# Kernel optimization log

Measured on AMD Instinct MI355X. Metric: run time of the kernel, lower is better.

Reference implementation:

```python
import jax, jax.numpy as jnp
import numpy as np

H = 1        # hidden_size: torch code branches `if c_0 > 0`, so state is scalar
SPIN = 365   # spinLen
TRAIN = 5000 # traintimeLen
ML = 2.9086
SL = 1.898


def setup_inputs() -> dict:
    key = jax.random.key(0)
    ks = jax.random.split(key, 13)
    B, S, I = 100000, 1, 2
    return {
        "x": jax.random.uniform(ks[0], (B, S, I), dtype=jnp.float32),
        "y_obs": jax.random.uniform(ks[1], (B, 1), dtype=jnp.float32),
        "p_mean": jax.random.uniform(ks[2], (1,), dtype=jnp.float32),
        "p_std": jnp.ones((1,), jnp.float32),
        "weight_r_yom": jax.random.uniform(ks[3], (H, H), dtype=jnp.float32),
        "weight_r_yom_gw": jax.random.uniform(ks[4], (H, H), dtype=jnp.float32),
        "weight_r_ylm": jax.random.uniform(ks[5], (H, H), dtype=jnp.float32),
        "weight_r_yfm": jax.random.uniform(ks[6], (H, H), dtype=jnp.float32),
        "bias_b0_yom": jax.random.uniform(ks[7], (H,), dtype=jnp.float32),
        "weight_b1_yom": jax.random.uniform(ks[8], (H, H), dtype=jnp.float32),
        "bias_b0_yom_gw": jax.random.uniform(ks[9], (H,), dtype=jnp.float32),
        "weight_b1_yom_gw": jax.random.uniform(ks[10], (H, H), dtype=jnp.float32),
        "bias_b0_ylm": jax.random.uniform(ks[11], (H,), dtype=jnp.float32),
        "weight_b2_ylm": jax.random.uniform(ks[12], (H, H), dtype=jnp.float32),
        "epoch": 1,
        "time_lag": 0,
    }


def _forward(x, y_obs, p_mean, p_std,
             weight_r_yom, weight_r_yom_gw, weight_r_ylm, weight_r_yfm,
             bias_b0_yom, weight_b1_yom, bias_b0_yom_gw, weight_b1_yom_gw,
             bias_b0_ylm, weight_b2_ylm, time_lag):
    B, S, _ = x.shape
    # softmax-like weight ratios (step-independent, hoisted out of the loop)
    den = (jnp.exp(weight_r_yom) + jnp.exp(weight_r_yom_gw)
           + jnp.exp(weight_r_ylm) + jnp.exp(weight_r_yfm))
    oo1 = jnp.exp(weight_r_yom) / den      # [H,H]
    oogw1 = jnp.exp(weight_r_yom_gw) / den
    ol1 = jnp.exp(weight_r_ylm) / den
    obsstd = jnp.std(y_obs[SPIN:TRAIN], ddof=1)  # torch.std is unbiased

    # step order in torch: b outer, t inner over x_orig[b, t] (batch_first)
    xs = x[time_lag:].reshape(-1, x.shape[-1])  # [(B-tl)*S, 2]

    def step(c0, u):                        # c0: [1,H]
        u1 = jnp.full((1, H), u[0])         # inflow
        u2 = jnp.full((1, H), u[1])         # PET
        z = (c0 - p_mean) / p_std
        oo = oo1 * jax.nn.sigmoid(bias_b0_yom + z @ weight_b1_yom)
        oogw = oogw1 * jax.nn.sigmoid(bias_b0_yom_gw + z @ weight_b1_yom_gw)
        ol = ol1 * jax.nn.sigmoid(bias_b0_ylm + ((u2 - ML) / SL) @ weight_b2_ylm)
        pos = c0 > 0
        ol_c = jnp.where(pos, ol - jax.nn.relu(ol - u2 / jnp.where(pos, c0, 1.0)), ol)
        f = 1.0 - oo - oogw - ol_c
        c1 = f * c0 + u1                    # ib = 0 => full inflow, bp = 0
        outs = (oo * c0, c0, ol * c0, ol_c * c0, oogw * c0, oo, ol, ol_c, f, oogw)
        return c1, outs

    c0 = jnp.zeros((1, H), x.dtype)
    _, outs = jax.lax.scan(step, c0, xs)

    def per_b(o):  # keep last-t value per b; zero-pad the skipped time_lag rows
        o = o.reshape(B - time_lag, S, 1, H)[:, -1, 0]
        return jnp.concatenate([jnp.zeros((time_lag, H), o.dtype), o], axis=0)

    h_n, c_n, l_n, lc_n, gw_n, g_oo, g_ol, g_olc, g_f, g_oogw = map(per_b, outs)
    zeros = jnp.zeros((B, H), x.dtype)
    bp_n = zeros      # ib = 0 always
    g_ib = zeros
    mask = jnp.concatenate([jnp.zeros((time_lag, H), x.dtype),
                            jnp.ones((B - time_lag, H), x.dtype)], axis=0)
    obs_std = obsstd * mask
    h_nout = jnp.concatenate([h_n, obs_std], axis=1)
    return (h_n, c_n, l_n, lc_n, bp_n, gw_n, g_ib, g_oo, g_ol, g_olc, g_f,
            g_oogw, h_nout, obs_std)


def reference(x, y_obs, p_mean, p_std, weight_r_yom, weight_r_yom_gw,
              weight_r_ylm, weight_r_yfm, bias_b0_yom, weight_b1_yom,
              bias_b0_yom_gw, weight_b1_yom_gw, bias_b0_ylm, weight_b2_ylm,
              epoch, time_lag):
    return _forward(x, y_obs, p_mean, p_std, weight_r_yom, weight_r_yom_gw,
                    weight_r_ylm, weight_r_yfm, bias_b0_yom, weight_b1_yom,
                    bias_b0_yom_gw, weight_b1_yom_gw, bias_b0_ylm,
                    weight_b2_ylm, time_lag)
```

## Files before the change

### kernel.cpp

```cpp
#include <hip/hip_runtime.h>
#include <math.h>


#define SPIN  365
#define TRAIN 5000
#define CHUNK 4
#define WARM  48
#define PF    4
#define BLK   128
#define SPAN  (BLK * CHUNK)
#define TLEN  (SPAN + WARM)
#define TSTR  140

#define F4BASE (SPIN - 1)
#define NF4    ((TRAIN - F4BASE) / 4)
#define SITER  ((NF4 + BLK - 1) / BLK)

#define MLc 2.9086f
#define SLc 1.898f

__device__ __forceinline__ float exp2a(float x) {
    float r; asm("v_exp_f32 %0, %1" : "=v"(r) : "v"(x)); return r;
}
__device__ __forceinline__ float rcpa(float x) {
    float r; asm("v_rcp_f32 %0, %1" : "=v"(r) : "v"(x)); return r;
}

__global__ void __launch_bounds__(BLK)
scan_kernel(const float* __restrict__ x, const float* __restrict__ y,
            const float* __restrict__ p_mean, const float* __restrict__ p_std,
            const float* __restrict__ w_r_yom, const float* __restrict__ w_r_yom_gw,
            const float* __restrict__ w_r_ylm, const float* __restrict__ w_r_yfm,
            const float* __restrict__ b0_yom, const float* __restrict__ w_b1_yom,
            const float* __restrict__ b0_yom_gw, const float* __restrict__ w_b1_yom_gw,
            const float* __restrict__ b0_ylm, const float* __restrict__ w_b2_ylm,
            const int* __restrict__ tlp, float* __restrict__ out, int B) {
    __shared__ __align__(128) float4 tile4[TLEN];
    __shared__ float sred[4];

    const int tid = threadIdx.x;
    const int tl = *tlp;
    const int N = B - tl;
    const size_t Bs = (size_t)B;

    const int blkbase = blockIdx.x * SPAN;
    const bool active = (blkbase < N);

    float2 sx[(TLEN + BLK - 1) / BLK];
    if (active) {
        const int T0 = blkbase - WARM;
        const float2* xp = (const float2*)x + tl;
        const int Nm1 = N - 1;
#pragma unroll
        for (int n = 0; n < (TLEN + BLK - 1) / BLK; ++n) {
            const int k = n * BLK + tid;
            const int g = min(max(T0 + min(k, TLEN - 1), 0), Nm1);
            sx[n] = xp[g];
        }
    }

    float4 yv[SITER];
    {
        const float4* y4 = (const float4*)(y + F4BASE);
#pragma unroll
        for (int n = 0; n < SITER; ++n)
            yv[n] = y4[min(n * BLK + tid, NF4 - 1)];
    }

    for (int r = blockIdx.x * BLK + tid; r < tl; r += gridDim.x * BLK) {
#pragma unroll
        for (int p = 0; p < 12; ++p) out[p * Bs + r] = 0.0f;
        out[12 * Bs + 2 * (size_t)r] = 0.0f;
        out[12 * Bs + 2 * (size_t)r + 1] = 0.0f;
        out[14 * Bs + r] = 0.0f;
    }

    const float pm = p_mean[0], inv_ps = 1.0f / p_std[0];
    const float ea = __expf(w_r_yom[0]);
    const float eb = __expf(w_r_yom_gw[0]);
    const float ec = __expf(w_r_ylm[0]);
    const float ed = __expf(w_r_yfm[0]);
    const float iden = 1.0f / (ea + eb + ec + ed);
    const float oo1 = ea * iden, oogw1 = eb * iden, ol1 = ec * iden;
    const float oo1g = oo1 + oogw1;
    const float LOG2E = 1.4426950408889634f;
    const float m1 = w_b1_yom[0]    * inv_ps, k1 = b0_yom[0]    - pm * m1;
    const float m2 = w_b1_yom_gw[0] * inv_ps, k2 = b0_yom_gw[0] - pm * m2;
    const float m3 = w_b2_ylm[0] * (1.0f / SLc), k3 = b0_ylm[0] - MLc * m3;
    const float A1 = -k1 * LOG2E, M1 = -m1 * LOG2E;
    const float A2 = -k2 * LOG2E, M2 = -m2 * LOG2E;
    const float A3 = -k3 * LOG2E, M3 = -m3 * LOG2E;

    if (active) {
#pragma unroll
        for (int n = 0; n < (TLEN + BLK - 1) / BLK; ++n) {
            const int k = n * BLK + tid;
            if (k < TLEN) {
                const float2 u = sx[n];
                const float olv = ol1 * rcpa(1.0f + exp2a(fmaf(u.y, M3, A3)));
                tile4[(k & 3) * TSTR + (k >> 2)] = make_float4(u.x, olv, u.y, 0.0f);
            }
        }
    }
    __syncthreads();

    float vh[CHUNK], vcc[CHUNK], vl[CHUNK], vlc[CHUNK], vgw[CHUNK];
    float voo[CHUNK], vol[CHUNK], volc[CHUNK], vf[CHUNK], vgg[CHUNK];
    const int i = tid;
    const int s0g = blkbase + i * CHUNK;

    if (active) {
        const int W0 = min(s0g, WARM);
        int qa = (i * CHUNK + (WARM - W0)) >> 2;

        float c = 0.0f;
        float4 bu[PF];
#pragma unroll
        for (int d = 0; d < PF; ++d) bu[d] = tile4[qa + TSTR * d];

        for (int w = 0; w < W0; w += PF) {
            ++qa;
#pragma unroll
            for (int d = 0; d < PF; ++d) {
                const float u1 = bu[d].x, olv = bu[d].y, u2 = bu[d].z;
                bu[d] = tile4[qa + TSTR * d];
                const float e1 = exp2a(fmaf(c, M1, A1));
                const float e2 = exp2a(fmaf(c, M2, A2));
                const float num = fmaf(oo1, e2, fmaf(oogw1, e1, oo1g));
                const float den = (1.0f + e1) * (1.0f + e2);
                const float r   = rcpa(den);
                const float lc  = fminf(olv * c, u2);
                const float t   = (c + u1) - lc;
                c = fmaf(-(num * c), r, t);
            }
        }

#pragma unroll
        for (int j = 0; j < CHUNK; ++j) {
            const float u1 = bu[j].x, olv = bu[j].y, u2 = bu[j].z;
            const float e1 = exp2a(fmaf(c, M1, A1));
            const float e2 = exp2a(fmaf(c, M2, A2));
            const float p1 = 1.0f + e1, p2 = 1.0f + e2;
            const float r  = rcpa(p1 * p2);
            const float oo   = oo1   * (p2 * r);
            const float oogw = oogw1 * (p1 * r);
            const float lc   = fminf(olv * c, u2);
            const float qq   = u2 * rcpa(c);
            const float olc  = (c > 0.0f) ? fminf(olv, qq) : olv;
            vh[j]  = oo * c;   vcc[j] = c;        vl[j]  = olv * c;
            vlc[j] = lc;       vgw[j] = oogw * c; voo[j] = oo;
            vol[j] = olv;      volc[j] = olc;     vgg[j] = oogw;
            vf[j]  = 1.0f - oo - oogw - olc;
            c = fmaf(-(oo + oogw), c, (c + u1) - lc);
        }
    }

    {
        float a0 = 0.f, a1 = 0.f, a2 = 0.f, a3 = 0.f;
        float q0 = 0.f, q1 = 0.f, q2 = 0.f, q3 = 0.f;
#pragma unroll
        for (int n = 0; n < SITER; ++n) {
            const int idx = n * BLK + tid;
            const float4 v = yv[n];
            const bool ok = (idx < NF4);
            const float d0 = (ok && idx != 0) ? v.x : 0.0f;
            const float d1 = ok ? v.y : 0.0f;
            const float d2 = ok ? v.z : 0.0f;
            const float d3 = ok ? v.w : 0.0f;
            a0 += d0; a1 += d1; a2 += d2; a3 += d3;
            q0 = fmaf(d0, d0, q0); q1 = fmaf(d1, d1, q1);
            q2 = fmaf(d2, d2, q2); q3 = fmaf(d3, d3, q3);
        }
        float a = (a0 + a1) + (a2 + a3);
        float q = (q0 + q1) + (q2 + q3);
#pragma unroll
        for (int m = 32; m > 0; m >>= 1) {
            a += __shfl_xor(a, m, 64);
            q += __shfl_xor(q, m, 64);
        }
        if ((tid & 63) == 0) {
            sred[(tid >> 6) * 2]     = a;
            sred[(tid >> 6) * 2 + 1] = q;
        }
    }
    __syncthreads();

    if (active && s0g < N) {
        const float A = sred[0] + sred[2];
        const float Q = sred[1] + sred[3];
        const float nn = (float)(TRAIN - SPIN);
        const float sd = sqrtf((Q - A * A / nn) / (nn - 1.0f));

        float* o_h    = out;
        float* o_c    = out + 1 * Bs;
        float* o_l    = out + 2 * Bs;
        float* o_lc   = out + 3 * Bs;
        float* o_bp   = out + 4 * Bs;
        float* o_gw   = out + 5 * Bs;
        float* o_gib  = out + 6 * Bs;
        float* o_goo  = out + 7 * Bs;
        float* o_gol  = out + 8 * Bs;
        float* o_golc = out + 9 * Bs;
        float* o_gf   = out + 10 * Bs;
        float* o_gogw = out + 11 * Bs;
        float* o_hno  = out + 12 * Bs;
        float* o_std  = out + 14 * Bs;
        const int b0 = tl + s0g;

        if (s0g + CHUNK <= N) {
            *(float4*)(o_h    + b0) = make_float4(vh[0],  vh[1],  vh[2],  vh[3]);
            *(float4*)(o_c    + b0) = make_float4(vcc[0], vcc[1], vcc[2], vcc[3]);
            *(float4*)(o_l    + b0) = make_float4(vl[0],  vl[1],  vl[2],  vl[3]);
            *(float4*)(o_lc   + b0) = make_float4(vlc[0], vlc[1], vlc[2], vlc[3]);
            *(float4*)(o_bp   + b0) = make_float4(0.f, 0.f, 0.f, 0.f);
            *(float4*)(o_gw   + b0) = make_float4(vgw[0], vgw[1], vgw[2], vgw[3]);
            *(float4*)(o_gib  + b0) = make_float4(0.f, 0.f, 0.f, 0.f);
            *(float4*)(o_goo  + b0) = make_float4(voo[0], voo[1], voo[2], voo[3]);
            *(float4*)(o_gol  + b0) = make_float4(vol[0], vol[1], vol[2], vol[3]);
            *(float4*)(o_golc + b0) = make_float4(volc[0],volc[1],volc[2],volc[3]);
            *(float4*)(o_gf   + b0) = make_float4(vf[0],  vf[1],  vf[2],  vf[3]);
            *(float4*)(o_gogw + b0) = make_float4(vgg[0], vgg[1], vgg[2], vgg[3]);
            *(float4*)(o_hno + 2 * (size_t)b0)     = make_float4(vh[0], sd, vh[1], sd);
            *(float4*)(o_hno + 2 * (size_t)b0 + 4) = make_float4(vh[2], sd, vh[3], sd);
            *(float4*)(o_std  + b0) = make_float4(sd, sd, sd, sd);
        } else {
            const int nrem = N - s0g;
#pragma unroll
            for (int j = 0; j < CHUNK; ++j) {
                if (j < nrem) {
                    const int b = b0 + j;
                    o_h[b]    = vh[j];   o_c[b]   = vcc[j];
                    o_l[b]    = vl[j];   o_lc[b]  = vlc[j];
                    o_bp[b]   = 0.0f;    o_gw[b]  = vgw[j];
                    o_gib[b]  = 0.0f;    o_goo[b] = voo[j];
                    o_gol[b]  = vol[j];  o_golc[b] = volc[j];
                    o_gf[b]   = vf[j];   o_gogw[b] = vgg[j];
                    o_hno[2 * (size_t)b]     = vh[j];
                    o_hno[2 * (size_t)b + 1] = sd;
                    o_std[b]  = sd;
                }
            }
        }
    }
}

extern "C" void kernel_launch(void* const* d_in, const int* in_sizes, int n_in,
                              void* d_out, int out_size, void* d_ws, size_t ws_size,
                              hipStream_t stream) {
    const float* x          = (const float*)d_in[0];
    const float* y_obs      = (const float*)d_in[1];
    const float* p_mean     = (const float*)d_in[2];
    const float* p_std      = (const float*)d_in[3];
    const float* w_r_yom    = (const float*)d_in[4];
    const float* w_r_yom_gw = (const float*)d_in[5];
    const float* w_r_ylm    = (const float*)d_in[6];
    const float* w_r_yfm    = (const float*)d_in[7];
    const float* b0_yom     = (const float*)d_in[8];
    const float* w_b1_yom   = (const float*)d_in[9];
    const float* b0_yom_gw  = (const float*)d_in[10];
    const float* w_b1_yomgw = (const float*)d_in[11];
    const float* b0_ylm     = (const float*)d_in[12];
    const float* w_b2_ylm   = (const float*)d_in[13];
    const int*   tlp        = (const int*)d_in[15];

    float* out = (float*)d_out;
    const int B = in_sizes[1];
    const int nblocks = (B + SPAN - 1) / SPAN;

    hipLaunchKernelGGL(scan_kernel, dim3(nblocks), dim3(BLK), 0, stream,
                       x, y_obs, p_mean, p_std, w_r_yom, w_r_yom_gw, w_r_ylm,
                       w_r_yfm, b0_yom, w_b1_yom, b0_yom_gw, w_b1_yomgw,
                       b0_ylm, w_b2_ylm, tlp, out, B);
}
```

Before: 12.02 us.

## Split block into scan waves and a dedicated std-reduction wave

Raises the block to 192 threads. The first two waves run the chunked recurrence scan and a third wave alone loads y and computes the sum and sum-of-squares for the std, so that latency overlaps the scan instead of adding to it. Warm-up length also drops from 48 to 32 steps, which shortens each thread's serial warm-up chain but gives the state less distance to converge. The dedicated wave adds register and occupancy cost.

```diff
diff --git a/kernel.cpp b/kernel.cpp
--- a/kernel.cpp
+++ b/kernel.cpp
@@ -5,16 +5,18 @@
 #define SPIN  365
 #define TRAIN 5000
 #define CHUNK 4
-#define WARM  48
+#define WARM  32
 #define PF    4
-#define BLK   128
-#define SPAN  (BLK * CHUNK)
+#define NSCAN 128
+#define BLK   192
+#define SPAN  (NSCAN * CHUNK)
 #define TLEN  (SPAN + WARM)
-#define TSTR  140
+#define TSTR  (TLEN / 4)
+#define SITN  ((TLEN + BLK - 1) / BLK)
 
 #define F4BASE (SPIN - 1)
 #define NF4    ((TRAIN - F4BASE) / 4)
-#define SITER  ((NF4 + BLK - 1) / BLK)
+#define SITER2 ((NF4 + 63) / 64)
 
 #define MLc 2.9086f
 #define SLc 1.898f
@@ -36,7 +38,7 @@
             const float* __restrict__ b0_ylm, const float* __restrict__ w_b2_ylm,
             const int* __restrict__ tlp, float* __restrict__ out, int B) {
     __shared__ __align__(128) float4 tile4[TLEN];
-    __shared__ float sred[4];
+    __shared__ float sred[2];
 
     const int tid = threadIdx.x;
     const int tl = *tlp;
@@ -46,25 +48,25 @@
     const int blkbase = blockIdx.x * SPAN;
     const bool active = (blkbase < N);
 
-    float2 sx[(TLEN + BLK - 1) / BLK];
+    float2 sx[SITN];
     if (active) {
         const int T0 = blkbase - WARM;
         const float2* xp = (const float2*)x + tl;
         const int Nm1 = N - 1;
 #pragma unroll
-        for (int n = 0; n < (TLEN + BLK - 1) / BLK; ++n) {
-            const int k = n * BLK + tid;
-            const int g = min(max(T0 + min(k, TLEN - 1), 0), Nm1);
-            sx[n] = xp[g];
-        }
-    }
-
-    float4 yv[SITER];
-    {
+        for (int n = 0; n < SITN; ++n) {
+            const int k = min(n * BLK + tid, TLEN - 1);
+            sx[n] = xp[min(max(T0 + k, 0), Nm1)];
+        }
+    }
+
+    float4 yv[SITER2];
+    if (tid >= NSCAN) {
+        const int lane = tid - NSCAN;
         const float4* y4 = (const float4*)(y + F4BASE);
 #pragma unroll
-        for (int n = 0; n < SITER; ++n)
-            yv[n] = y4[min(n * BLK + tid, NF4 - 1)];
+        for (int n = 0; n < SITER2; ++n)
+            yv[n] = y4[min(n * 64 + lane, NF4 - 1)];
     }
 
     for (int r = blockIdx.x * BLK + tid; r < tl; r += gridDim.x * BLK) {
@@ -93,7 +95,7 @@
 
     if (active) {
 #pragma unroll
-        for (int n = 0; n < (TLEN + BLK - 1) / BLK; ++n) {
+        for (int n = 0; n < SITN; ++n) {
             const int k = n * BLK + tid;
             if (k < TLEN) {
                 const float2 u = sx[n];
@@ -106,61 +108,61 @@
 
     float vh[CHUNK], vcc[CHUNK], vl[CHUNK], vlc[CHUNK], vgw[CHUNK];
     float voo[CHUNK], vol[CHUNK], volc[CHUNK], vf[CHUNK], vgg[CHUNK];
-    const int i = tid;
-    const int s0g = blkbase + i * CHUNK;
-
-    if (active) {
-        const int W0 = min(s0g, WARM);
-        int qa = (i * CHUNK + (WARM - W0)) >> 2;
-
-        float c = 0.0f;
-        float4 bu[PF];
-#pragma unroll
-        for (int d = 0; d < PF; ++d) bu[d] = tile4[qa + TSTR * d];
-
-        for (int w = 0; w < W0; w += PF) {
-            ++qa;
-#pragma unroll
-            for (int d = 0; d < PF; ++d) {
-                const float u1 = bu[d].x, olv = bu[d].y, u2 = bu[d].z;
-                bu[d] = tile4[qa + TSTR * d];
+    const int s0g = blkbase + tid * CHUNK;
+
+    if (tid < NSCAN) {
+        if (active) {
+            const int W0 = min(s0g, WARM);
+            int qa = (tid * CHUNK + (WARM - W0)) >> 2;
+
+            float c = 0.0f;
+            float4 bu[PF];
+#pragma unroll
+            for (int d = 0; d < PF; ++d) bu[d] = tile4[qa + TSTR * d];
+
+            for (int w = 0; w < W0; w += PF) {
+                ++qa;
+#pragma unroll
+                for (int d = 0; d < PF; ++d) {
+                    const float u1 = bu[d].x, olv = bu[d].y, u2 = bu[d].z;
+                    bu[d] = tile4[qa + TSTR * d];
+                    const float e1 = exp2a(fmaf(c, M1, A1));
+                    const float e2 = exp2a(fmaf(c, M2, A2));
+                    const float num = fmaf(oo1, e2, fmaf(oogw1, e1, oo1g));
+                    const float den = (1.0f + e1) * (1.0f + e2);
+                    const float r   = rcpa(den);
+                    const float lc  = fminf(olv * c, u2);
+                    const float t   = (c + u1) - lc;
+                    c = fmaf(-(num * c), r, t);
+                }
+            }
+
+#pragma unroll
+            for (int j = 0; j < CHUNK; ++j) {
+                const float u1 = bu[j].x, olv = bu[j].y, u2 = bu[j].z;
                 const float e1 = exp2a(fmaf(c, M1, A1));
                 const float e2 = exp2a(fmaf(c, M2, A2));
-                const float num = fmaf(oo1, e2, fmaf(oogw1, e1, oo1g));
-                const float den = (1.0f + e1) * (1.0f + e2);
-                const float r   = rcpa(den);
-                const float lc  = fminf(olv * c, u2);
-                const float t   = (c + u1) - lc;
-                c = fmaf(-(num * c), r, t);
-            }
-        }
-
-#pragma unroll
-        for (int j = 0; j < CHUNK; ++j) {
-            const float u1 = bu[j].x, olv = bu[j].y, u2 = bu[j].z;
-            const float e1 = exp2a(fmaf(c, M1, A1));
-            const float e2 = exp2a(fmaf(c, M2, A2));
-            const float p1 = 1.0f + e1, p2 = 1.0f + e2;
-            const float r  = rcpa(p1 * p2);
-            const float oo   = oo1   * (p2 * r);
-            const float oogw = oogw1 * (p1 * r);
-            const float lc   = fminf(olv * c, u2);
-            const float qq   = u2 * rcpa(c);
-            const float olc  = (c > 0.0f) ? fminf(olv, qq) : olv;
-            vh[j]  = oo * c;   vcc[j] = c;        vl[j]  = olv * c;
-            vlc[j] = lc;       vgw[j] = oogw * c; voo[j] = oo;
-            vol[j] = olv;      volc[j] = olc;     vgg[j] = oogw;
-            vf[j]  = 1.0f - oo - oogw - olc;
-            c = fmaf(-(oo + oogw), c, (c + u1) - lc);
-        }
-    }
-
-    {
+                const float p1 = 1.0f + e1, p2 = 1.0f + e2;
+                const float r  = rcpa(p1 * p2);
+                const float oo   = oo1   * (p2 * r);
+                const float oogw = oogw1 * (p1 * r);
+                const float lc   = fminf(olv * c, u2);
+                const float qq   = u2 * rcpa(c);
+                const float olc  = (c > 0.0f) ? fminf(olv, qq) : olv;
+                vh[j]  = oo * c;   vcc[j] = c;        vl[j]  = olv * c;
+                vlc[j] = lc;       vgw[j] = oogw * c; voo[j] = oo;
+                vol[j] = olv;      volc[j] = olc;     vgg[j] = oogw;
+                vf[j]  = 1.0f - oo - oogw - olc;
+                c = fmaf(-(oo + oogw), c, (c + u1) - lc);
+            }
+        }
+    } else {
+        const int lane = tid - NSCAN;
         float a0 = 0.f, a1 = 0.f, a2 = 0.f, a3 = 0.f;
         float q0 = 0.f, q1 = 0.f, q2 = 0.f, q3 = 0.f;
 #pragma unroll
-        for (int n = 0; n < SITER; ++n) {
-            const int idx = n * BLK + tid;
+        for (int n = 0; n < SITER2; ++n) {
+            const int idx = n * 64 + lane;
             const float4 v = yv[n];
             const bool ok = (idx < NF4);
             const float d0 = (ok && idx != 0) ? v.x : 0.0f;
@@ -178,16 +180,12 @@
             a += __shfl_xor(a, m, 64);
             q += __shfl_xor(q, m, 64);
         }
-        if ((tid & 63) == 0) {
-            sred[(tid >> 6) * 2]     = a;
-            sred[(tid >> 6) * 2 + 1] = q;
-        }
+        if (lane == 0) { sred[0] = a; sred[1] = q; }
     }
     __syncthreads();
 
-    if (active && s0g < N) {
-        const float A = sred[0] + sred[2];
-        const float Q = sred[1] + sred[3];
+    if (tid < NSCAN && active && s0g < N) {
+        const float A = sred[0], Q = sred[1];
         const float nn = (float)(TRAIN - SPIN);
         const float sd = sqrtf((Q - A * A / nn) / (nn - 1.0f));
 
```

Result: slower. 16.33 us (+35.9%).
